# Kernel optimization log

Measured on AMD Instinct MI355X. Metric: run time of the kernel, lower is better.

## Reference

```python
import jax, jax.numpy as jnp
import numpy as np

SIG = [1, 1, 1, 1, -1]  # Cl(4,1)
GA_DIM = 1 << len(SIG)  # 32
IN_F, OUT_F = 128, 128
EPS = 1e-6


def _cayley(sig):
    """Dense Cayley tensor C[a,b,k]: e_a * e_b = C[a,b,a^b] * e_{a^b}.
    Only dim^2 of the dim^3 entries are nonzero (one k per (a,b))."""
    n = len(sig)
    dim = 1 << n
    C = np.zeros((dim, dim, dim), dtype=np.float32)
    for a in range(dim):
        for b in range(dim):
            # reordering sign from moving b's generators past a's
            s = 0
            aa = a >> 1
            while aa:
                s += bin(aa & b).count('1')
                aa >>= 1
            sign = -1.0 if (s & 1) else 1.0
            # metric contribution from repeated generators
            common = a & b
            for i in range(n):
                if common & (1 << i):
                    sign *= sig[i]
            C[a, b, a ^ b] = sign
    return C

_C = jnp.asarray(_cayley(SIG))  # [32,32,32]


def setup_inputs() -> dict:
    key = jax.random.key(0)
    kx, kw = jax.random.split(key)
    x = jax.random.normal(kx, (4096, IN_F, GA_DIM), dtype=jnp.float32)
    std = (2.0 / (IN_F * GA_DIM)) ** 0.5
    w = jax.random.normal(kw, (OUT_F, IN_F, GA_DIM), dtype=jnp.float32) * std
    return {"x": x, "weight": w}


def reference(x, weight):
    # Fold Cayley table into the weight once: Wc[o,f,i,k] = sum_j W[o,f,j] C[i,j,k]
    Wc = jnp.einsum('ofj,ijk->ofik', weight, _C)
    # Geometric linear layer: y[b,o,k] = sum_{f,i} x[b,f,i] Wc[o,f,i,k]
    y = jnp.einsum('bfi,ofik->bok', x, Wc)
    # Manifold normalization: project each output multivector to unit norm
    inv = jax.lax.rsqrt(jnp.sum(y * y, axis=-1, keepdims=True) + EPS)
    return y * inv
```

## Files before the change

kernel.cpp:

```cpp
#include <hip/hip_runtime.h>
#include <stdint.h>

typedef unsigned short ushort_t;
typedef __attribute__((ext_vector_type(8))) __bf16 bf16x8;
typedef __attribute__((ext_vector_type(4))) float  f32x4;


__device__ __forceinline__ unsigned int f2bf(float f) {
    unsigned int u = __float_as_uint(f);
    return (u + 0x7FFFu + ((u >> 16) & 1u)) >> 16;
}

__device__ __forceinline__ float cayley_sign(int a, int b) {
    int s = 0;
    int aa = a >> 1;
    while (aa) { s += __popc(aa & b); aa >>= 1; }
    float sign = (s & 1) ? -1.0f : 1.0f;
    if (a & b & 16) sign = -sign;
    return sign;
}

__device__ __forceinline__ void async16(const ushort_t* g, const ushort_t* l) {
    const __attribute__((address_space(1))) unsigned int* gp =
        (const __attribute__((address_space(1))) unsigned int*)(uintptr_t)g;
    __attribute__((address_space(3))) unsigned int* lp =
        (__attribute__((address_space(3))) unsigned int*)(unsigned int)(uintptr_t)l;
    __builtin_amdgcn_global_load_lds(gp, lp, 16, 0, 0);
}

__global__ __launch_bounds__(256) void prepAB(const float* __restrict__ x,
                                              const float* __restrict__ w,
                                              ushort_t* __restrict__ A_sw,
                                              ushort_t* __restrict__ B_sw) {
    const int k_blk = blockIdx.x;
    const int p_blk = blockIdx.y >> 1;
    const int sub   = blockIdx.y & 1;
    const int t = threadIdx.x;
    const int r  = sub * 64 + (t >> 2);
    const int kq = t & 3;

    const int kt = k_blk >> 1;
    const int kh = k_blk & 1;

    if (blockIdx.z == 0) {
        const int R = p_blk * 128 + r;
        const float* src = x + (size_t)R * 4096 + (size_t)k_blk * 32 + kq * 8;
        float4 a = ((const float4*)src)[0];
        float4 b = ((const float4*)src)[1];
        uint4 pk;
        pk.x = f2bf(a.x) | (f2bf(a.y) << 16);
        pk.y = f2bf(a.z) | (f2bf(a.w) << 16);
        pk.z = f2bf(b.x) | (f2bf(b.y) << 16);
        pk.w = f2bf(b.z) | (f2bf(b.w) << 16);
        const int P = R >> 8, rowp = R & 255;
        *(uint4*)(A_sw + (size_t)(P * 64 + kt) * 16384 + kh * 8192 + kq * 2048 + rowp * 8) = pk;
    } else {
        const int n = p_blk * 128 + r;
        const int o = n >> 5;
        const int kc = n & 31;
        const float* wrow = w + (size_t)o * 4096 + (size_t)k_blk * 32;
        unsigned int pk[4];
#pragma unroll
        for (int pr = 0; pr < 4; ++pr) {
            const int i0 = kq * 8 + pr * 2, i1 = i0 + 1;
            const int j0 = i0 ^ kc, j1 = i1 ^ kc;
            float v0 = wrow[j0] * cayley_sign(i0, j0);
            float v1 = wrow[j1] * cayley_sign(i1, j1);
            pk[pr] = f2bf(v0) | (f2bf(v1) << 16);
        }
        uint4 u = {pk[0], pk[1], pk[2], pk[3]};
        const int P = n >> 8, colp = n & 255;
        *(uint4*)(B_sw + (size_t)(P * 64 + kt) * 16384 + kh * 8192 + kq * 2048 + colp * 8) = u;
    }
}


#define MFMA16(a, b, c) __builtin_amdgcn_mfma_f32_16x16x32_bf16(a, b, c, 0, 0, 0)

#define BLOAD(OFS) do {                                                        \
        bF[0] = *(const bf16x8*)(Bc + bOff + (OFS) + 0 * 128);                 \
        bF[1] = *(const bf16x8*)(Bc + bOff + (OFS) + 1 * 128);                 \
        bF[2] = *(const bf16x8*)(Bc + bOff + (OFS) + 2 * 128);                 \
        bF[3] = *(const bf16x8*)(Bc + bOff + (OFS) + 3 * 128);                 \
    } while (0)

#define GA_PHASE(TMB, KH, PRE_STMT, STAGE_STMT, TAIL_STMT)                     \
    {                                                                          \
        PRE_STMT;                                                              \
        const ushort_t* ap_ = Ac + aOff + (KH) * 8192 + (TMB) * 128;           \
        bf16x8 aF0 = *(const bf16x8*)(ap_ + 0 * 128);                          \
        bf16x8 aF1 = *(const bf16x8*)(ap_ + 1 * 128);                          \
        bf16x8 aF2 = *(const bf16x8*)(ap_ + 2 * 128);                          \
        bf16x8 aF3 = *(const bf16x8*)(ap_ + 3 * 128);                          \
        STAGE_STMT;                                                            \
        __builtin_amdgcn_s_barrier();                                          \
        asm volatile("s_waitcnt lgkmcnt(0)" ::: "memory");                     \
        __builtin_amdgcn_s_setprio(1);                                         \
        acc[(TMB) + 0][0] = MFMA16(aF0, bF[0], acc[(TMB) + 0][0]);             \
        acc[(TMB) + 0][1] = MFMA16(aF0, bF[1], acc[(TMB) + 0][1]);             \
        acc[(TMB) + 0][2] = MFMA16(aF0, bF[2], acc[(TMB) + 0][2]);             \
        acc[(TMB) + 0][3] = MFMA16(aF0, bF[3], acc[(TMB) + 0][3]);             \
        acc[(TMB) + 1][0] = MFMA16(aF1, bF[0], acc[(TMB) + 1][0]);             \
        acc[(TMB) + 1][1] = MFMA16(aF1, bF[1], acc[(TMB) + 1][1]);             \
        acc[(TMB) + 1][2] = MFMA16(aF1, bF[2], acc[(TMB) + 1][2]);             \
        acc[(TMB) + 1][3] = MFMA16(aF1, bF[3], acc[(TMB) + 1][3]);             \
        acc[(TMB) + 2][0] = MFMA16(aF2, bF[0], acc[(TMB) + 2][0]);             \
        acc[(TMB) + 2][1] = MFMA16(aF2, bF[1], acc[(TMB) + 2][1]);             \
        acc[(TMB) + 2][2] = MFMA16(aF2, bF[2], acc[(TMB) + 2][2]);             \
        acc[(TMB) + 2][3] = MFMA16(aF2, bF[3], acc[(TMB) + 2][3]);             \
        acc[(TMB) + 3][0] = MFMA16(aF3, bF[0], acc[(TMB) + 3][0]);             \
        acc[(TMB) + 3][1] = MFMA16(aF3, bF[1], acc[(TMB) + 3][1]);             \
        acc[(TMB) + 3][2] = MFMA16(aF3, bF[2], acc[(TMB) + 3][2]);             \
        acc[(TMB) + 3][3] = MFMA16(aF3, bF[3], acc[(TMB) + 3][3]);             \
        __builtin_amdgcn_s_setprio(0);                                         \
        TAIL_STMT;                                                             \
        __builtin_amdgcn_s_barrier();                                          \
    }

__global__ __launch_bounds__(512, 2) void gemm_norm(const ushort_t* __restrict__ A_sw,
                                                    const ushort_t* __restrict__ B_sw,
                                                    float* __restrict__ out) {
    __shared__ ushort_t As[2][16384];
    __shared__ ushort_t Bs[2][16384];

    int id = blockIdx.x;
    id = (id & 7) * 32 + (id >> 3);
    const int m_blk = id >> 4;
    const int n_blk = id & 15;

    const int t    = threadIdx.x;
    const int wave = t >> 6;
    const int lane = t & 63;
    const int wr = wave >> 2;
    const int wc = wave & 3;
    const int lg = lane >> 4;
    const int lm = lane & 15;

    const int aOff = (lg * 256 + wr * 128 + lm) * 8;
    const int bOff = (lg * 256 + wc * 64  + lm) * 8;

    const ushort_t* aPanel = A_sw + (size_t)m_blk * 64 * 16384;
    const ushort_t* bPanel = B_sw + (size_t)n_blk * 64 * 16384;

    f32x4 acc[8][4];
#pragma unroll
    for (int i = 0; i < 8; ++i)
#pragma unroll
        for (int j = 0; j < 4; ++j)
#pragma unroll
            for (int k = 0; k < 4; ++k) acc[i][j][k] = 0.0f;

    const int so = wave * 1024 + lane * 8;
    const int sl = wave * 1024;

    auto STAGE2 = [&](const ushort_t* src, const ushort_t* ldsb) {
        async16(src + so,       ldsb + sl);
        async16(src + so + 512, ldsb + sl + 512);
    };

    const int NT = 64;

    STAGE2(bPanel + 0,            &Bs[0][0]);
    STAGE2(bPanel + 8192,         &Bs[0][8192]);
    STAGE2(aPanel + 0,            &As[0][0]);
    STAGE2(aPanel + 8192,         &As[0][8192]);
    STAGE2(bPanel + 16384,        &Bs[1][0]);
    STAGE2(bPanel + 16384 + 8192, &Bs[1][8192]);
    asm volatile("s_waitcnt vmcnt(4)" ::: "memory");
    __builtin_amdgcn_s_barrier();

#pragma unroll 2
    for (int tt = 0; tt < NT; ++tt) {
        const int b = tt & 1;
        const ushort_t* Ac = &As[b][0];
        const ushort_t* Bc = &Bs[b][0];
        ushort_t* An = &As[b ^ 1][0];
        ushort_t* Bn = &Bs[b][0];

        bf16x8 bF[4];

        GA_PHASE(0, 0, BLOAD(0),
                 if (tt + 1 < NT) STAGE2(aPanel + (size_t)(tt + 1) * 16384, An),
                 {})
        GA_PHASE(4, 0, {},
                 if (tt + 1 < NT) STAGE2(aPanel + (size_t)(tt + 1) * 16384 + 8192, An + 8192),
                 {})
        GA_PHASE(0, 1, BLOAD(8192),
                 if (tt + 2 < NT) STAGE2(bPanel + (size_t)(tt + 2) * 16384, Bn),
                 {})
        GA_PHASE(4, 1, {},
                 if (tt + 2 < NT) STAGE2(bPanel + (size_t)(tt + 2) * 16384 + 8192, Bn + 8192),
                 { if (tt < NT - 2)       asm volatile("s_waitcnt vmcnt(4)" ::: "memory");
                   else if (tt == NT - 2) asm volatile("s_waitcnt vmcnt(0)" ::: "memory"); })
    }

    const int row0 = m_blk * 256 + wr * 128;
    const int col0 = n_blk * 256 + wc * 64;
#pragma unroll
    for (int tm = 0; tm < 8; ++tm) {
#pragma unroll
        for (int u = 0; u < 2; ++u) {
#pragma unroll
            for (int reg = 0; reg < 4; ++reg) {
                float v0 = acc[tm][2 * u][reg];
                float v1 = acc[tm][2 * u + 1][reg];
                float p = v0 * v0 + v1 * v1;
                p += __shfl_xor(p, 1);
                p += __shfl_xor(p, 2);
                p += __shfl_xor(p, 4);
                p += __shfl_xor(p, 8);
                const float inv = rsqrtf(p + 1e-6f);
                const int row = row0 + tm * 16 + lg * 4 + reg;
                float* orow = out + (size_t)row * 4096 + col0 + u * 32 + lm;
                orow[0]  = v0 * inv;
                orow[16] = v1 * inv;
            }
        }
    }
}


extern "C" void kernel_launch(void* const* d_in, const int* in_sizes, int n_in,
                              void* d_out, int out_size, void* d_ws, size_t ws_size,
                              hipStream_t stream) {
    const float* x = (const float*)d_in[0];
    const float* w = (const float*)d_in[1];
    float* out = (float*)d_out;

    ushort_t* A_sw = (ushort_t*)d_ws;
    ushort_t* B_sw = A_sw + (size_t)4096 * 4096;

    prepAB<<<dim3(128, 64, 2), 256, 0, stream>>>(x, w, A_sw, B_sw);
    gemm_norm<<<dim3(256), 512, 0, stream>>>(A_sw, B_sw, out);
}
```

Before: 230.7 us.

## Deepen async prefetch pipeline with peeled epilogue iterations

Reorders the global-to-LDS async staging so the A panel for the next-next tile is prefetched earlier and more loads are in flight (vmcnt(10) instead of vmcnt(4)). The last two K iterations are peeled out of the main loop, which removes the per-iteration bounds checks and lets the drain use tailored waitcnts. The intent is to hide more global memory latency behind MFMA work. The cost is more outstanding loads and a more intricate buffer-reuse schedule, where a wrong wait count or overlapping buffer write would corrupt results.

New measurement: 230.4 us. About the same (-0.1%).

```diff
diff --git a/kernel.cpp b/kernel.cpp
--- a/kernel.cpp
+++ b/kernel.cpp
@@ -153,45 +153,67 @@
     const int so = wave * 1024 + lane * 8;
     const int sl = wave * 1024;
 
-    auto STAGE2 = [&](const ushort_t* src, const ushort_t* ldsb) {
+    auto STAGE2 = [&](const ushort_t* src, ushort_t* ldsb) {
         async16(src + so,       ldsb + sl);
         async16(src + so + 512, ldsb + sl + 512);
     };
 
     const int NT = 64;
 
-    STAGE2(bPanel + 0,            &Bs[0][0]);
-    STAGE2(bPanel + 8192,         &Bs[0][8192]);
-    STAGE2(aPanel + 0,            &As[0][0]);
-    STAGE2(aPanel + 8192,         &As[0][8192]);
-    STAGE2(bPanel + 16384,        &Bs[1][0]);
-    STAGE2(bPanel + 16384 + 8192, &Bs[1][8192]);
-    asm volatile("s_waitcnt vmcnt(4)" ::: "memory");
+    STAGE2(bPanel + 0,             &Bs[0][0]);
+    STAGE2(aPanel + 0,             &As[0][0]);
+    STAGE2(bPanel + 8192,          &Bs[0][8192]);
+    STAGE2(aPanel + 8192,          &As[0][8192]);
+    STAGE2(bPanel + 16384,         &Bs[1][0]);
+    STAGE2(aPanel + 16384,         &As[1][0]);
+    STAGE2(bPanel + 16384 + 8192,  &Bs[1][8192]);
+    asm volatile("s_waitcnt vmcnt(10)" ::: "memory");
     __builtin_amdgcn_s_barrier();
 
 #pragma unroll 2
-    for (int tt = 0; tt < NT; ++tt) {
+    for (int tt = 0; tt < NT - 2; ++tt) {
         const int b = tt & 1;
         const ushort_t* Ac = &As[b][0];
         const ushort_t* Bc = &Bs[b][0];
-        ushort_t* An = &As[b ^ 1][0];
-        ushort_t* Bn = &Bs[b][0];
 
         bf16x8 bF[4];
 
         GA_PHASE(0, 0, BLOAD(0),
-                 if (tt + 1 < NT) STAGE2(aPanel + (size_t)(tt + 1) * 16384, An),
+                 STAGE2(aPanel + (size_t)(tt + 1) * 16384 + 8192, &As[b ^ 1][8192]),
                  {})
         GA_PHASE(4, 0, {},
-                 if (tt + 1 < NT) STAGE2(aPanel + (size_t)(tt + 1) * 16384 + 8192, An + 8192),
-                 {})
+                 STAGE2(bPanel + (size_t)(tt + 2) * 16384, &Bs[b][0]),
+                 asm volatile("s_waitcnt vmcnt(10)" ::: "memory"))
         GA_PHASE(0, 1, BLOAD(8192),
-                 if (tt + 2 < NT) STAGE2(bPanel + (size_t)(tt + 2) * 16384, Bn),
+                 STAGE2(aPanel + (size_t)(tt + 2) * 16384, &As[b][0]),
                  {})
         GA_PHASE(4, 1, {},
-                 if (tt + 2 < NT) STAGE2(bPanel + (size_t)(tt + 2) * 16384 + 8192, Bn + 8192),
-                 { if (tt < NT - 2)       asm volatile("s_waitcnt vmcnt(4)" ::: "memory");
-                   else if (tt == NT - 2) asm volatile("s_waitcnt vmcnt(0)" ::: "memory"); })
+                 STAGE2(bPanel + (size_t)(tt + 2) * 16384 + 8192, &Bs[b][8192]),
+                 asm volatile("s_waitcnt vmcnt(10)" ::: "memory"))
+    }
+
+    {
+        const ushort_t* Ac = &As[0][0];
+        const ushort_t* Bc = &Bs[0][0];
+        bf16x8 bF[4];
+        GA_PHASE(0, 0, BLOAD(0),
+                 STAGE2(aPanel + (size_t)(NT - 1) * 16384 + 8192, &As[1][8192]),
+                 {})
+        GA_PHASE(4, 0, {}, {},
+                 asm volatile("s_waitcnt vmcnt(8)" ::: "memory"))
+        GA_PHASE(0, 1, BLOAD(8192), {}, {})
+        GA_PHASE(4, 1, {}, {},
+                 asm volatile("s_waitcnt vmcnt(4)" ::: "memory"))
+    }
+    {
+        const ushort_t* Ac = &As[1][0];
+        const ushort_t* Bc = &Bs[1][0];
+        bf16x8 bF[4];
+        GA_PHASE(0, 0, BLOAD(0), {}, {})
+        GA_PHASE(4, 0, {}, {},
+                 asm volatile("s_waitcnt vmcnt(0)" ::: "memory"))
+        GA_PHASE(0, 1, BLOAD(8192), {}, {})
+        GA_PHASE(4, 1, {}, {}, {})
     }
 
     const int row0 = m_blk * 256 + wr * 128;
```

## Switch GEMM to 32x32x16 MFMA with register double-buffered LDS reads

Applied to the files above, without the earlier changes.

Replaces the 16x16x32 bf16 MFMA tiling with 32x32x16 MFMAs, reorganising the accumulators and LDS read offsets to match. Fragment reads from LDS are double-buffered in registers (x/y sets) so the reads for the next sub-step are issued before the current MFMAs, with fewer barriers per K tile. The prefetch schedule is also changed to stage A and B halves in alternating order, with a peeled epilogue for the last two tiles. The norm epilogue now reduces over 32 lanes. This risks wrong results if the swizzled layout does not match the new fragment mapping, and adds register pressure.

Measured after the change: 244.2 us. +5.8%, slower.

```diff
diff --git a/kernel.cpp b/kernel.cpp
--- a/kernel.cpp
+++ b/kernel.cpp
@@ -2,8 +2,8 @@
 #include <stdint.h>
 
 typedef unsigned short ushort_t;
-typedef __attribute__((ext_vector_type(8))) __bf16 bf16x8;
-typedef __attribute__((ext_vector_type(4))) float  f32x4;
+typedef __attribute__((ext_vector_type(8)))  __bf16 bf16x8;
+typedef __attribute__((ext_vector_type(16))) float  f32x16;
 
 
 __device__ __forceinline__ unsigned int f2bf(float f) {
@@ -75,47 +75,32 @@
 }
 
 
-#define MFMA16(a, b, c) __builtin_amdgcn_mfma_f32_16x16x32_bf16(a, b, c, 0, 0, 0)
-
-#define BLOAD(OFS) do {                                                        \
-        bF[0] = *(const bf16x8*)(Bc + bOff + (OFS) + 0 * 128);                 \
-        bF[1] = *(const bf16x8*)(Bc + bOff + (OFS) + 1 * 128);                 \
-        bF[2] = *(const bf16x8*)(Bc + bOff + (OFS) + 2 * 128);                 \
-        bF[3] = *(const bf16x8*)(Bc + bOff + (OFS) + 3 * 128);                 \
+#define MFMA32(a, b, c) __builtin_amdgcn_mfma_f32_32x32x16_bf16(a, b, c, 0, 0, 0)
+
+#define RD_SET(A0, A1, A2, A3, Bv0, Bv1, ABASE, BBASE, SOFS) do {              \
+        const ushort_t* _pa = (ABASE) + aBase + (SOFS);                        \
+        A0 = *(const bf16x8*)(_pa);                                            \
+        A1 = *(const bf16x8*)(_pa + 256);                                      \
+        A2 = *(const bf16x8*)(_pa + 512);                                      \
+        A3 = *(const bf16x8*)(_pa + 768);                                      \
+        const ushort_t* _pb = (BBASE) + bBase + (SOFS);                        \
+        Bv0 = *(const bf16x8*)(_pb);                                           \
+        Bv1 = *(const bf16x8*)(_pb + 256);                                     \
     } while (0)
 
-#define GA_PHASE(TMB, KH, PRE_STMT, STAGE_STMT, TAIL_STMT)                     \
-    {                                                                          \
-        PRE_STMT;                                                              \
-        const ushort_t* ap_ = Ac + aOff + (KH) * 8192 + (TMB) * 128;           \
-        bf16x8 aF0 = *(const bf16x8*)(ap_ + 0 * 128);                          \
-        bf16x8 aF1 = *(const bf16x8*)(ap_ + 1 * 128);                          \
-        bf16x8 aF2 = *(const bf16x8*)(ap_ + 2 * 128);                          \
-        bf16x8 aF3 = *(const bf16x8*)(ap_ + 3 * 128);                          \
-        STAGE_STMT;                                                            \
-        __builtin_amdgcn_s_barrier();                                          \
-        asm volatile("s_waitcnt lgkmcnt(0)" ::: "memory");                     \
+#define MFMA_SET(A0, A1, A2, A3, Bv0, Bv1)                                     \
         __builtin_amdgcn_s_setprio(1);                                         \
-        acc[(TMB) + 0][0] = MFMA16(aF0, bF[0], acc[(TMB) + 0][0]);             \
-        acc[(TMB) + 0][1] = MFMA16(aF0, bF[1], acc[(TMB) + 0][1]);             \
-        acc[(TMB) + 0][2] = MFMA16(aF0, bF[2], acc[(TMB) + 0][2]);             \
-        acc[(TMB) + 0][3] = MFMA16(aF0, bF[3], acc[(TMB) + 0][3]);             \
-        acc[(TMB) + 1][0] = MFMA16(aF1, bF[0], acc[(TMB) + 1][0]);             \
-        acc[(TMB) + 1][1] = MFMA16(aF1, bF[1], acc[(TMB) + 1][1]);             \
-        acc[(TMB) + 1][2] = MFMA16(aF1, bF[2], acc[(TMB) + 1][2]);             \
-        acc[(TMB) + 1][3] = MFMA16(aF1, bF[3], acc[(TMB) + 1][3]);             \
-        acc[(TMB) + 2][0] = MFMA16(aF2, bF[0], acc[(TMB) + 2][0]);             \
-        acc[(TMB) + 2][1] = MFMA16(aF2, bF[1], acc[(TMB) + 2][1]);             \
-        acc[(TMB) + 2][2] = MFMA16(aF2, bF[2], acc[(TMB) + 2][2]);             \
-        acc[(TMB) + 2][3] = MFMA16(aF2, bF[3], acc[(TMB) + 2][3]);             \
-        acc[(TMB) + 3][0] = MFMA16(aF3, bF[0], acc[(TMB) + 3][0]);             \
-        acc[(TMB) + 3][1] = MFMA16(aF3, bF[1], acc[(TMB) + 3][1]);             \
-        acc[(TMB) + 3][2] = MFMA16(aF3, bF[2], acc[(TMB) + 3][2]);             \
-        acc[(TMB) + 3][3] = MFMA16(aF3, bF[3], acc[(TMB) + 3][3]);             \
-        __builtin_amdgcn_s_setprio(0);                                         \
-        TAIL_STMT;                                                             \
-        __builtin_amdgcn_s_barrier();                                          \
-    }
+        acc[0][0] = MFMA32(A0, Bv0, acc[0][0]);                                \
+        acc[0][1] = MFMA32(A0, Bv1, acc[0][1]);                                \
+        acc[1][0] = MFMA32(A1, Bv0, acc[1][0]);                                \
+        acc[1][1] = MFMA32(A1, Bv1, acc[1][1]);                                \
+        acc[2][0] = MFMA32(A2, Bv0, acc[2][0]);                                \
+        acc[2][1] = MFMA32(A2, Bv1, acc[2][1]);                                \
+        acc[3][0] = MFMA32(A3, Bv0, acc[3][0]);                                \
+        acc[3][1] = MFMA32(A3, Bv1, acc[3][1]);                                \
+        __builtin_amdgcn_s_setprio(0);
+
+#define SBAR0() __builtin_amdgcn_sched_barrier(0)
 
 __global__ __launch_bounds__(512, 2) void gemm_norm(const ushort_t* __restrict__ A_sw,
                                                     const ushort_t* __restrict__ B_sw,
@@ -133,87 +118,147 @@
     const int lane = t & 63;
     const int wr = wave >> 2;
     const int wc = wave & 3;
-    const int lg = lane >> 4;
-    const int lm = lane & 15;
-
-    const int aOff = (lg * 256 + wr * 128 + lm) * 8;
-    const int bOff = (lg * 256 + wc * 64  + lm) * 8;
+    const int half = lane >> 5;
+    const int l32  = lane & 31;
+
+    const int aBase = half * 2048 + (wr * 128 + l32) * 8;
+    const int bBase = half * 2048 + (wc * 64 + l32) * 8;
 
     const ushort_t* aPanel = A_sw + (size_t)m_blk * 64 * 16384;
     const ushort_t* bPanel = B_sw + (size_t)n_blk * 64 * 16384;
 
-    f32x4 acc[8][4];
-#pragma unroll
-    for (int i = 0; i < 8; ++i)
-#pragma unroll
-        for (int j = 0; j < 4; ++j)
-#pragma unroll
-            for (int k = 0; k < 4; ++k) acc[i][j][k] = 0.0f;
+    f32x16 acc[4][2];
+#pragma unroll
+    for (int i = 0; i < 4; ++i)
+#pragma unroll
+        for (int j = 0; j < 2; ++j)
+#pragma unroll
+            for (int k = 0; k < 16; ++k) acc[i][j][k] = 0.0f;
 
     const int so = wave * 1024 + lane * 8;
     const int sl = wave * 1024;
 
-    auto STAGE2 = [&](const ushort_t* src, const ushort_t* ldsb) {
+    auto STAGE2 = [&](const ushort_t* src, ushort_t* ldsb) {
         async16(src + so,       ldsb + sl);
         async16(src + so + 512, ldsb + sl + 512);
     };
 
     const int NT = 64;
 
+    STAGE2(aPanel + 0,            &As[0][0]);
     STAGE2(bPanel + 0,            &Bs[0][0]);
+    STAGE2(aPanel + 8192,         &As[0][8192]);
     STAGE2(bPanel + 8192,         &Bs[0][8192]);
-    STAGE2(aPanel + 0,            &As[0][0]);
-    STAGE2(aPanel + 8192,         &As[0][8192]);
+    STAGE2(aPanel + 16384,        &As[1][0]);
     STAGE2(bPanel + 16384,        &Bs[1][0]);
-    STAGE2(bPanel + 16384 + 8192, &Bs[1][8192]);
     asm volatile("s_waitcnt vmcnt(4)" ::: "memory");
     __builtin_amdgcn_s_barrier();
 
+    bf16x8 xa0, xa1, xa2, xa3, xb0, xb1;
+    bf16x8 ya0, ya1, ya2, ya3, yb0, yb1;
+
+    RD_SET(xa0, xa1, xa2, xa3, xb0, xb1, &As[0][0], &Bs[0][0], 0);
+
 #pragma unroll 2
-    for (int tt = 0; tt < NT; ++tt) {
+    for (int tt = 0; tt < NT - 2; ++tt) {
         const int b = tt & 1;
         const ushort_t* Ac = &As[b][0];
         const ushort_t* Bc = &Bs[b][0];
         ushort_t* An = &As[b ^ 1][0];
-        ushort_t* Bn = &Bs[b][0];
-
-        bf16x8 bF[4];
-
-        GA_PHASE(0, 0, BLOAD(0),
-                 if (tt + 1 < NT) STAGE2(aPanel + (size_t)(tt + 1) * 16384, An),
-                 {})
-        GA_PHASE(4, 0, {},
-                 if (tt + 1 < NT) STAGE2(aPanel + (size_t)(tt + 1) * 16384 + 8192, An + 8192),
-                 {})
-        GA_PHASE(0, 1, BLOAD(8192),
-                 if (tt + 2 < NT) STAGE2(bPanel + (size_t)(tt + 2) * 16384, Bn),
-                 {})
-        GA_PHASE(4, 1, {},
-                 if (tt + 2 < NT) STAGE2(bPanel + (size_t)(tt + 2) * 16384 + 8192, Bn + 8192),
-                 { if (tt < NT - 2)       asm volatile("s_waitcnt vmcnt(4)" ::: "memory");
-                   else if (tt == NT - 2) asm volatile("s_waitcnt vmcnt(0)" ::: "memory"); })
+        ushort_t* Bn = &Bs[b ^ 1][0];
+
+        STAGE2(aPanel + (size_t)(tt + 1) * 16384 + 8192, An + 8192);
+        RD_SET(ya0, ya1, ya2, ya3, yb0, yb1, Ac, Bc, 4096);
+        SBAR0();
+        MFMA_SET(xa0, xa1, xa2, xa3, xb0, xb1)
+
+        STAGE2(bPanel + (size_t)(tt + 1) * 16384 + 8192, Bn + 8192);
+        RD_SET(xa0, xa1, xa2, xa3, xb0, xb1, Ac, Bc, 8192);
+        SBAR0();
+        MFMA_SET(ya0, ya1, ya2, ya3, yb0, yb1)
+        asm volatile("s_waitcnt vmcnt(4)" ::: "memory");
+        __builtin_amdgcn_s_barrier();
+
+        STAGE2(aPanel + (size_t)(tt + 2) * 16384, &As[b][0]);
+        RD_SET(ya0, ya1, ya2, ya3, yb0, yb1, Ac, Bc, 12288);
+        SBAR0();
+        MFMA_SET(xa0, xa1, xa2, xa3, xb0, xb1)
+
+        STAGE2(bPanel + (size_t)(tt + 2) * 16384, &Bs[b][0]);
+        RD_SET(xa0, xa1, xa2, xa3, xb0, xb1, An, Bn, 0);
+        SBAR0();
+        MFMA_SET(ya0, ya1, ya2, ya3, yb0, yb1)
+        asm volatile("s_waitcnt vmcnt(4)" ::: "memory");
+        __builtin_amdgcn_s_barrier();
+    }
+
+    {
+        const ushort_t* Ac = &As[0][0];
+        const ushort_t* Bc = &Bs[0][0];
+        ushort_t* An = &As[1][0];
+        ushort_t* Bn = &Bs[1][0];
+
+        STAGE2(aPanel + (size_t)(NT - 1) * 16384 + 8192, An + 8192);
+        RD_SET(ya0, ya1, ya2, ya3, yb0, yb1, Ac, Bc, 4096);
+        SBAR0();
+        MFMA_SET(xa0, xa1, xa2, xa3, xb0, xb1)
+
+        STAGE2(bPanel + (size_t)(NT - 1) * 16384 + 8192, Bn + 8192);
+        RD_SET(xa0, xa1, xa2, xa3, xb0, xb1, Ac, Bc, 8192);
+        SBAR0();
+        MFMA_SET(ya0, ya1, ya2, ya3, yb0, yb1)
+        asm volatile("s_waitcnt vmcnt(4)" ::: "memory");
+        __builtin_amdgcn_s_barrier();
+
+        RD_SET(ya0, ya1, ya2, ya3, yb0, yb1, Ac, Bc, 12288);
+        SBAR0();
+        MFMA_SET(xa0, xa1, xa2, xa3, xb0, xb1)
+
+        RD_SET(xa0, xa1, xa2, xa3, xb0, xb1, An, Bn, 0);
+        SBAR0();
+        MFMA_SET(ya0, ya1, ya2, ya3, yb0, yb1)
+        asm volatile("s_waitcnt vmcnt(0)" ::: "memory");
+        __builtin_amdgcn_s_barrier();
+    }
+    {
+        const ushort_t* Ac = &As[1][0];
+        const ushort_t* Bc = &Bs[1][0];
+
+        RD_SET(ya0, ya1, ya2, ya3, yb0, yb1, Ac, Bc, 4096);
+        SBAR0();
+        MFMA_SET(xa0, xa1, xa2, xa3, xb0, xb1)
+
+        RD_SET(xa0, xa1, xa2, xa3, xb0, xb1, Ac, Bc, 8192);
+        SBAR0();
+        MFMA_SET(ya0, ya1, ya2, ya3, yb0, yb1)
+
+        RD_SET(ya0, ya1, ya2, ya3, yb0, yb1, Ac, Bc, 12288);
+        SBAR0();
+        MFMA_SET(xa0, xa1, xa2, xa3, xb0, xb1)
+
+        SBAR0();
+        MFMA_SET(ya0, ya1, ya2, ya3, yb0, yb1)
     }
 
     const int row0 = m_blk * 256 + wr * 128;
     const int col0 = n_blk * 256 + wc * 64;
 #pragma unroll
-    for (int tm = 0; tm < 8; ++tm) {
-#pragma unroll
-        for (int u = 0; u < 2; ++u) {
-#pragma unroll
-            for (int reg = 0; reg < 4; ++reg) {
-                float v0 = acc[tm][2 * u][reg];
-                float v1 = acc[tm][2 * u + 1][reg];
-                float p = v0 * v0 + v1 * v1;
+    for (int tm = 0; tm < 4; ++tm) {
+#pragma unroll
+        for (int tn = 0; tn < 2; ++tn) {
+            const int cbase = col0 + tn * 32 + l32;
+#pragma unroll
+            for (int reg = 0; reg < 16; ++reg) {
+                float v = acc[tm][tn][reg];
+                float p = v * v;
                 p += __shfl_xor(p, 1);
                 p += __shfl_xor(p, 2);
                 p += __shfl_xor(p, 4);
                 p += __shfl_xor(p, 8);
+                p += __shfl_xor(p, 16);
                 const float inv = rsqrtf(p + 1e-6f);
-                const int row = row0 + tm * 16 + lg * 4 + reg;
-                float* orow = out + (size_t)row * 4096 + col0 + u * 32 + lm;
-                orow[0]  = v0 * inv;
-                orow[16] = v1 * inv;
+                const int row = row0 + tm * 32 + (reg & 3) + 8 * (reg >> 2) + 4 * half;
+                out[(size_t)row * 4096 + cbase] = v * inv;
             }
         }
     }
@@ -231,5 +276,5 @@
     ushort_t* B_sw = A_sw + (size_t)4096 * 4096;
 
     prepAB<<<dim3(128, 64, 2), 256, 0, stream>>>(x, w, A_sw, B_sw);
-    gemm_norm<<<dim3(256), 512, 0, stream>>>(A_sw, B_sw, out);
-}
+    gemm_norm<<<dim3(32 * 8), 512, 0, stream>>>(A_sw, B_sw, out);
+}
```
